# Kernel optimization log

Hardware: AMD Instinct MI355X
Metric: run time of the kernel (lower is better)

## Reference

```python
import jax, jax.numpy as jnp
import numpy as np

NUM_HEADS = 8
EPS = 1e-6


def setup_inputs() -> dict:
    key = jax.random.key(0)
    ks = jax.random.split(key, 6)
    B, C, H, W = 32, 512, 32, 32
    E = C
    scale = 1.0 / np.sqrt(E)
    x = jax.random.normal(ks[0], (B, C, H, W), dtype=jnp.float32)
    Wq = jax.random.normal(ks[1], (E, E), dtype=jnp.float32) * scale
    Wk = jax.random.normal(ks[2], (E, E), dtype=jnp.float32) * scale
    Wv = jax.random.normal(ks[3], (E, E), dtype=jnp.float32) * scale
    Wo = jax.random.normal(ks[4], (E, E), dtype=jnp.float32) * scale
    bo = jnp.zeros((E,), dtype=jnp.float32)
    return {"x": x, "Wq": Wq, "Wk": Wk, "Wv": Wv, "Wo": Wo, "bo": bo}


def reference(x, Wq, Wk, Wv, Wo, bo):
    B, C, H, W = x.shape
    S = H * W
    nh = NUM_HEADS
    hd = C // nh
    # (B, C, H, W) -> (B, S, C)
    t = x.reshape(B, C, S).transpose(0, 2, 1)
    # torch Linear: t @ W.T  (no bias for q/k/v)
    Q = (t @ Wq.T).reshape(B, S, nh, hd).transpose(0, 2, 1, 3)  # (B, nh, S, hd)
    K = (t @ Wk.T).reshape(B, S, nh, hd).transpose(0, 2, 1, 3)
    V = (t @ Wv.T).reshape(B, S, nh, hd).transpose(0, 2, 1, 3)
    phi_Q = jax.nn.elu(Q) + 1.0
    phi_K = jax.nn.elu(K) + 1.0
    # K^T V aggregation: (B, nh, hd, hd)
    KV = jnp.einsum('bhsd,bhse->bhde', phi_K, V)
    numerator = jnp.einsum('bhsd,bhde->bhse', phi_Q, KV)      # (B, nh, S, hd)
    # phi_K^T @ ones == sum over seq: (B, nh, hd)
    k_sum = jnp.sum(phi_K, axis=2)
    denominator = jnp.einsum('bhsd,bhd->bhs', phi_Q, k_sum)[..., None]  # (B, nh, S, 1)
    out = numerator / (denominator + EPS)
    out = out.transpose(0, 2, 1, 3).reshape(B, S, C)          # (B, S, C)
    out = out @ Wo.T + bo
    out = out.transpose(0, 2, 1).reshape(B, C, H, W)
    return out
```

## Files before the change

### kernel.cpp

```cpp
#include <hip/hip_runtime.h>
#include <hip/hip_bf16.h>

typedef __bf16 bf16;
typedef __bf16 bf16x2 __attribute__((ext_vector_type(2)));
typedef __bf16 bf16x4 __attribute__((ext_vector_type(4)));
typedef __bf16 bf16x8 __attribute__((ext_vector_type(8)));
typedef float  f32x4  __attribute__((ext_vector_type(4)));

#define MFMA16(a,b,c) __builtin_amdgcn_mfma_f32_16x16x32_bf16((a),(b),(c),0,0,0)

constexpr int Cn = 512;
constexpr int Sn = 1024;

__device__ __forceinline__ void bar_lds() {
    asm volatile("s_waitcnt lgkmcnt(0)" ::: "memory");
    __builtin_amdgcn_sched_barrier(0);
    __builtin_amdgcn_s_barrier();
}

__global__ __launch_bounds__(256) void k_cvt_w(const float* __restrict__ Wq,
                                               const float* __restrict__ Wk,
                                               const float* __restrict__ Wv,
                                               const float* __restrict__ Wo,
                                               bf16* __restrict__ Wb) {
    int tid = blockIdx.x * 256 + threadIdx.x;
    int oidx = tid * 8;
    int m  = oidx >> 18;
    int r  = oidx & 262143;
    int gr = r >> 13;
    int kc = (r >> 9) & 15;
    int l  = (r >> 3) & 63;
    const float* s = (m == 0) ? Wq : (m == 1) ? Wk : (m == 2) ? Wv : Wo;
    const float* src = s + (gr * 16 + (l & 15)) * 512 + kc * 32 + (l >> 4) * 8;
    float4 u = ((const float4*)src)[0], v = ((const float4*)src)[1];
    bf16x8 o;
    o[0] = (bf16)u.x; o[1] = (bf16)u.y; o[2] = (bf16)u.z; o[3] = (bf16)u.w;
    o[4] = (bf16)v.x; o[5] = (bf16)v.y; o[6] = (bf16)v.z; o[7] = (bf16)v.w;
    *(bf16x8*)(Wb + oidx) = o;
}

__global__ __launch_bounds__(1024, 4) void k_qkv(const float* __restrict__ x,
                                                 const bf16* __restrict__ Wb,
                                                 bf16* __restrict__ phiQ,
                                                 bf16* __restrict__ kvP,
                                                 float* __restrict__ ksP) {
    int bid = blockIdx.x;
    int st8 = bid & 7, b = bid >> 3;
    int t = threadIdx.x, lane = t & 63, w = t >> 6;
    int l15 = lane & 15, g = lane >> 4;
    int hq   = w >> 2;
    int quad = w & 3;

    __shared__ bf16 xT[64][520];
    __shared__ bf16 pk[4][64][72];
    __shared__ bf16 vv[4][64][72];
    __shared__ float ksl[512];

    if (t < 512) ksl[t] = 0.f;

    int rp = t >> 2;
    int sq = (t & 3) << 4;

    const float* xr0 = x + ((size_t)b * Cn + 2 * rp) * Sn + st8 * 128 + sq;
    {
        float4 f0[4], f1[4];
#pragma unroll
        for (int j = 0; j < 4; ++j) {
            f0[j] = ((const float4*)xr0)[j];
            f1[j] = ((const float4*)(xr0 + Sn))[j];
        }
#pragma unroll
        for (int j = 0; j < 4; ++j) {
            const float* e0 = (const float*)&f0[j];
            const float* e1 = (const float*)&f1[j];
#pragma unroll
            for (int e = 0; e < 4; ++e) {
                bf16x2 pr; pr[0] = (bf16)e0[e]; pr[1] = (bf16)e1[e];
                *(bf16x2*)&xT[sq + j * 4 + e][2 * rp] = pr;
            }
        }
    }
    float4 fB0[4], fB1[4];
#pragma unroll
    for (int j = 0; j < 4; ++j) {
        fB0[j] = ((const float4*)(xr0 + 64))[j];
        fB1[j] = ((const float4*)(xr0 + 64 + Sn))[j];
    }
    __syncthreads();

#pragma unroll 1
    for (int sub = 0; sub < 2; ++sub) {
        int srow0 = st8 * 128 + sub * 64;
#pragma unroll 1
        for (int rnd = 0; rnd < 2; ++rnd) {
            int h = rnd * 4 + hq;
            int gr = h * 4 + quad;
            f32x4 aQ[4], aK[4], aV[4];
#pragma unroll
            for (int n = 0; n < 4; ++n) {
                aQ[n] = (f32x4){0.f,0.f,0.f,0.f};
                aK[n] = (f32x4){0.f,0.f,0.f,0.f};
                aV[n] = (f32x4){0.f,0.f,0.f,0.f};
            }
            const bf16* wfQ = Wb + ((size_t)gr * 16) * 512 + lane * 8;
            const bf16* wfK = wfQ + (size_t)32 * 16 * 512;
            const bf16* wfV = wfQ + (size_t)64 * 16 * 512;
#pragma unroll 2
            for (int kc = 0; kc < 16; ++kc) {
                bf16x8 fq = *(const bf16x8*)(wfQ + kc * 512);
                bf16x8 fk = *(const bf16x8*)(wfK + kc * 512);
                bf16x8 fv = *(const bf16x8*)(wfV + kc * 512);
#pragma unroll
                for (int n = 0; n < 4; ++n) {
                    bf16x8 bf_ = *(const bf16x8*)&xT[n * 16 + l15][kc * 32 + g * 8];
                    aQ[n] = MFMA16(fq, bf_, aQ[n]);
                    aK[n] = MFMA16(fk, bf_, aK[n]);
                    aV[n] = MFMA16(fv, bf_, aV[n]);
                }
            }
            float kspart[4] = {0.f, 0.f, 0.f, 0.f};
#pragma unroll
            for (int n = 0; n < 4; ++n) {
                bf16x4 qv;
#pragma unroll
                for (int r = 0; r < 4; ++r) {
                    float kv_ = aK[n][r];
                    kv_ = kv_ > 0.f ? kv_ + 1.f : __expf(kv_);
                    bf16 kb = (bf16)kv_;
                    kspart[r] += (float)kb;
                    pk[hq][quad * 16 + g * 4 + r][n * 16 + l15] = kb;
                    vv[hq][quad * 16 + g * 4 + r][n * 16 + l15] = (bf16)aV[n][r];
                    float q = aQ[n][r];
                    q = q > 0.f ? q + 1.f : __expf(q);
                    qv[r] = (bf16)q;
                }
                *(bf16x4*)(phiQ + ((size_t)b * Sn + srow0 + n * 16 + l15) * Cn
                           + h * 64 + quad * 16 + g * 4) = qv;
            }
#pragma unroll
            for (int r = 0; r < 4; ++r) {
                float v = kspart[r];
                v += __shfl_xor(v, 1);
                v += __shfl_xor(v, 2);
                v += __shfl_xor(v, 4);
                v += __shfl_xor(v, 8);
                if (l15 == 0) ksl[h * 64 + quad * 16 + g * 4 + r] += v;
            }
            bar_lds();
            if (sub == 0 && rnd == 1) {
#pragma unroll
                for (int j = 0; j < 4; ++j) {
                    const float* e0 = (const float*)&fB0[j];
                    const float* e1 = (const float*)&fB1[j];
#pragma unroll
                    for (int e = 0; e < 4; ++e) {
                        bf16x2 pr; pr[0] = (bf16)e0[e]; pr[1] = (bf16)e1[e];
                        *(bf16x2*)&xT[sq + j * 4 + e][2 * rp] = pr;
                    }
                }
            }
            f32x4 kvacc[4];
#pragma unroll
            for (int n = 0; n < 4; ++n) kvacc[n] = (f32x4){0.f,0.f,0.f,0.f};
#pragma unroll
            for (int k2 = 0; k2 < 2; ++k2) {
                bf16x8 af = *(const bf16x8*)&pk[hq][quad * 16 + l15][k2 * 32 + g * 8];
#pragma unroll
                for (int n = 0; n < 4; ++n) {
                    bf16x8 bf_ = *(const bf16x8*)&vv[hq][n * 16 + l15][k2 * 32 + g * 8];
                    kvacc[n] = MFMA16(af, bf_, kvacc[n]);
                }
            }
            {
                bf16x8 p0, p1;
#pragma unroll
                for (int r = 0; r < 4; ++r) {
                    p0[r]     = (bf16)kvacc[0][r];
                    p0[4 + r] = (bf16)kvacc[1][r];
                    p1[r]     = (bf16)kvacc[2][r];
                    p1[4 + r] = (bf16)kvacc[3][r];
                }
                size_t base = ((size_t)((b * 8 + h) * 16 + st8 * 2 + sub)) * 4096;
                bf16* dst = kvP + base + (size_t)(quad * 64 + lane) * 16;
                *(bf16x8*)(dst)     = p0;
                *(bf16x8*)(dst + 8) = p1;
            }
            bar_lds();
        }
    }
    if (t < 512) {
        int h = t >> 6, d = t & 63;
        ksP[((b * 8 + h) * 8 + st8) * 64 + d] = ksl[t];
    }
}

__global__ __launch_bounds__(256) void k_red(const bf16* __restrict__ kvP,
                                             const float* __restrict__ ksP,
                                             bf16* __restrict__ KVT,
                                             float* __restrict__ ksum) {
    int bh = blockIdx.x;
    int t = threadIdx.x;
    int wq = t >> 6, lane = t & 63, g = lane >> 4, l15 = lane & 15;
    float acc[16];
#pragma unroll
    for (int i = 0; i < 16; ++i) acc[i] = 0.f;
#pragma unroll
    for (int p = 0; p < 16; ++p) {
        const bf16* src = kvP + ((size_t)bh * 16 + p) * 4096 + (size_t)t * 16;
        bf16x8 v0 = *(const bf16x8*)(src);
        bf16x8 v1 = *(const bf16x8*)(src + 8);
#pragma unroll
        for (int i = 0; i < 8; ++i) { acc[i] += (float)v0[i]; acc[8 + i] += (float)v1[i]; }
    }
#pragma unroll
    for (int n = 0; n < 4; ++n) {
        bf16x4 o;
#pragma unroll
        for (int r = 0; r < 4; ++r) o[r] = (bf16)acc[n * 4 + r];
        *(bf16x4*)(KVT + (size_t)bh * 4096 + (n * 16 + l15) * 64 + wq * 16 + g * 4) = o;
    }
    if (t < 64) {
        float s = 0.f;
#pragma unroll
        for (int p = 0; p < 8; ++p) s += ksP[((size_t)bh * 8 + p) * 64 + t];
        ksum[bh * 64 + t] = s;
    }
}

__global__ __launch_bounds__(1024, 4) void k_apply(const bf16* __restrict__ phiQ,
                                                   const bf16* __restrict__ Wb,
                                                   const bf16* __restrict__ KVT,
                                                   const float* __restrict__ ksum,
                                                   const float* __restrict__ bo,
                                                   float* __restrict__ out) {
    int bid = blockIdx.x;
    int st8 = bid & 7, b = bid >> 3;
    int t = threadIdx.x, lane = t & 63, w = t >> 6, l15 = lane & 15, g = lane >> 4;

    __shared__ bf16 pq[64][520];
    __shared__ float ksl[512];
    __shared__ float rden[64][8];
    __shared__ float bol[512];

    if (t < 512) {
        ksl[t] = ksum[b * 512 + t];
        bol[t] = bo[t];
    }

#pragma unroll 1
    for (int sub = 0; sub < 2; ++sub) {
        int srow0 = st8 * 128 + sub * 64;
        {
            int sr = t >> 4, c0 = (t & 15) * 32;
            const bf16* src = phiQ + ((size_t)b * Sn + srow0 + sr) * Cn + c0;
#pragma unroll
            for (int j = 0; j < 4; ++j)
                *(bf16x8*)&pq[sr][c0 + j * 8] = *(const bf16x8*)(src + j * 8);
        }
        __syncthreads();
        {
            int j = t >> 1, half = t & 1;
            int s = j & 63, h = j >> 6;
            float acc = 0.f;
#pragma unroll
            for (int dt = 0; dt < 4; ++dt) {
                bf16x8 v = *(const bf16x8*)&pq[s][h * 64 + half * 32 + dt * 8];
#pragma unroll
                for (int i = 0; i < 8; ++i)
                    acc += ksl[h * 64 + half * 32 + dt * 8 + i] * (float)v[i];
            }
            acc += __shfl_xor(acc, 1);
            if (half == 0) rden[s][h] = 1.f / (acc + 1e-6f);
        }
        __syncthreads();
        int h = w >> 1, eh = w & 1;
        f32x4 accN[2][4];
#pragma unroll
        for (int mi = 0; mi < 2; ++mi)
#pragma unroll
            for (int n = 0; n < 4; ++n) accN[mi][n] = (f32x4){0.f,0.f,0.f,0.f};
        {
            const bf16* kvb = KVT + ((size_t)(b * 8 + h)) * 4096;
#pragma unroll
            for (int k2 = 0; k2 < 2; ++k2) {
#pragma unroll
                for (int mi = 0; mi < 2; ++mi) {
                    bf16x8 af = *(const bf16x8*)(kvb + (eh * 32 + mi * 16 + l15) * 64 + k2 * 32 + g * 8);
#pragma unroll
                    for (int n = 0; n < 4; ++n) {
                        bf16x8 bf_ = *(const bf16x8*)&pq[n * 16 + l15][h * 64 + k2 * 32 + g * 8];
                        accN[mi][n] = MFMA16(af, bf_, accN[mi][n]);
                    }
                }
            }
        }
        __syncthreads();
#pragma unroll
        for (int mi = 0; mi < 2; ++mi)
#pragma unroll
            for (int n = 0; n < 4; ++n) {
                float rd = rden[n * 16 + l15][h];
                bf16x4 ov;
#pragma unroll
                for (int r = 0; r < 4; ++r) ov[r] = (bf16)(accN[mi][n][r] * rd);
                *(bf16x4*)&pq[n * 16 + l15][h * 64 + eh * 32 + mi * 16 + g * 4] = ov;
            }
        __syncthreads();
        int m0 = w * 32;
        f32x4 acc[2][4];
#pragma unroll
        for (int mi = 0; mi < 2; ++mi)
#pragma unroll
            for (int n = 0; n < 4; ++n) acc[mi][n] = (f32x4){0.f,0.f,0.f,0.f};
        const bf16* WoF = Wb + 786432 + (size_t)(w * 2) * 16 * 512 + lane * 8;
#pragma unroll 2
        for (int kc = 0; kc < 16; ++kc) {
            bf16x8 fa0 = *(const bf16x8*)(WoF + kc * 512);
            bf16x8 fa1 = *(const bf16x8*)(WoF + (16 + kc) * 512);
#pragma unroll
            for (int n = 0; n < 4; ++n) {
                bf16x8 bf_ = *(const bf16x8*)&pq[n * 16 + l15][kc * 32 + g * 8];
                acc[0][n] = MFMA16(fa0, bf_, acc[0][n]);
                acc[1][n] = MFMA16(fa1, bf_, acc[1][n]);
            }
        }
#pragma unroll
        for (int mi = 0; mi < 2; ++mi)
#pragma unroll
            for (int r = 0; r < 4; ++r) {
                int co = m0 + mi * 16 + g * 4 + r;
                float bb = bol[co];
#pragma unroll
                for (int n = 0; n < 4; ++n)
                    out[((size_t)b * Cn + co) * Sn + srow0 + n * 16 + l15] = acc[mi][n][r] + bb;
            }
        __syncthreads();
    }
}

extern "C" void kernel_launch(void* const* d_in, const int* in_sizes, int n_in,
                              void* d_out, int out_size, void* d_ws, size_t ws_size,
                              hipStream_t stream) {
    const float* x  = (const float*)d_in[0];
    const float* Wq = (const float*)d_in[1];
    const float* Wk = (const float*)d_in[2];
    const float* Wv = (const float*)d_in[3];
    const float* Wo = (const float*)d_in[4];
    const float* bo = (const float*)d_in[5];
    float* out = (float*)d_out;

    char* ws = (char*)d_ws;
    bf16*  phiQ = (bf16*)ws;
    bf16*  Wb   = (bf16*)(ws + 33554432);
    float* ksP  = (float*)(ws + 35651584);
    bf16*  KVT  = (bf16*)(ws + 36175872);
    float* ks   = (float*)(ws + 38273024);

    bf16*  kvP  = (bf16*)d_out;

    k_cvt_w <<< 512,  256, 0, stream>>>(Wq, Wk, Wv, Wo, Wb);
    k_qkv   <<< 256, 1024, 0, stream>>>(x, Wb, phiQ, kvP, ksP);
    k_red   <<< 256,  256, 0, stream>>>(kvP, ksP, KVT, ks);
    k_apply <<< 256, 1024, 0, stream>>>(phiQ, Wb, KVT, ks, bo, out);
}
```

Before: 116.0 us.

## Split QKV projection into smaller 512-thread blocks with swizzled LDS tiles

```diff
diff --git a/kernel.cpp b/kernel.cpp
--- a/kernel.cpp
+++ b/kernel.cpp
@@ -39,190 +39,187 @@
     *(bf16x8*)(Wb + oidx) = o;
 }
 
-__global__ __launch_bounds__(1024, 4) void k_qkv(const float* __restrict__ x,
-                                                 const bf16* __restrict__ Wb,
-                                                 bf16* __restrict__ phiQ,
-                                                 bf16* __restrict__ kvP,
-                                                 float* __restrict__ ksP) {
+__global__ __launch_bounds__(512, 4) void k_qkv(const float* __restrict__ x,
+                                                const bf16* __restrict__ Wb,
+                                                bf16* __restrict__ phiQ,
+                                                bf16* __restrict__ kvP,
+                                                float* __restrict__ ksP) {
     int bid = blockIdx.x;
-    int st8 = bid & 7, b = bid >> 3;
+    int st = bid & 15, b = bid >> 4;
     int t = threadIdx.x, lane = t & 63, w = t >> 6;
     int l15 = lane & 15, g = lane >> 4;
-    int hq   = w >> 2;
     int quad = w & 3;
-
-    __shared__ bf16 xT[64][520];
-    __shared__ bf16 pk[4][64][72];
-    __shared__ bf16 vv[4][64][72];
-    __shared__ float ksl[512];
-
-    if (t < 512) ksl[t] = 0.f;
-
-    int rp = t >> 2;
-    int sq = (t & 3) << 4;
-
-    const float* xr0 = x + ((size_t)b * Cn + 2 * rp) * Sn + st8 * 128 + sq;
+    int hh2  = w >> 2;
+
+    __shared__ bf16 xT[64 * 512];
+    __shared__ bf16 pkb[64 * 64];
+    __shared__ bf16 vvb[64 * 64];
+
     {
-        float4 f0[4], f1[4];
-#pragma unroll
-        for (int j = 0; j < 4; ++j) {
-            f0[j] = ((const float4*)xr0)[j];
-            f1[j] = ((const float4*)(xr0 + Sn))[j];
-        }
-#pragma unroll
-        for (int j = 0; j < 4; ++j) {
-            const float* e0 = (const float*)&f0[j];
-            const float* e1 = (const float*)&f1[j];
+        int rp = t >> 1;
+        int sh = (t & 1) * 32;
+        const float* xr = x + ((size_t)b * Cn + 2 * rp) * Sn + st * 64 + sh;
+#pragma unroll
+        for (int j = 0; j < 8; ++j) {
+            float4 a0 = ((const float4*)xr)[j];
+            float4 a1 = ((const float4*)(xr + Sn))[j];
+            const float* e0 = (const float*)&a0;
+            const float* e1 = (const float*)&a1;
 #pragma unroll
             for (int e = 0; e < 4; ++e) {
+                int s = sh + j * 4 + e;
                 bf16x2 pr; pr[0] = (bf16)e0[e]; pr[1] = (bf16)e1[e];
-                *(bf16x2*)&xT[sq + j * 4 + e][2 * rp] = pr;
-            }
-        }
-    }
-    float4 fB0[4], fB1[4];
-#pragma unroll
-    for (int j = 0; j < 4; ++j) {
-        fB0[j] = ((const float4*)(xr0 + 64))[j];
-        fB1[j] = ((const float4*)(xr0 + 64 + Sn))[j];
-    }
-    __syncthreads();
+                *(bf16x2*)&xT[s * 512 + (((rp >> 2) ^ (s & 7)) << 3) + 2 * (rp & 3)] = pr;
+            }
+        }
+    }
+    bar_lds();
 
 #pragma unroll 1
-    for (int sub = 0; sub < 2; ++sub) {
-        int srow0 = st8 * 128 + sub * 64;
+    for (int rnd = 0; rnd < 4; ++rnd) {
+        int h = rnd * 2 + hh2;
+        int gr = h * 4 + quad;
+        f32x4 aQ[4], aK[4], aV[4];
+#pragma unroll
+        for (int n = 0; n < 4; ++n) {
+            aQ[n] = (f32x4){0.f,0.f,0.f,0.f};
+            aK[n] = (f32x4){0.f,0.f,0.f,0.f};
+            aV[n] = (f32x4){0.f,0.f,0.f,0.f};
+        }
+        const bf16* wfQ = Wb + ((size_t)gr * 16) * 512 + lane * 8;
+        const bf16* wfK = wfQ + (size_t)32 * 16 * 512;
+        const bf16* wfV = wfQ + (size_t)64 * 16 * 512;
+#pragma unroll 2
+        for (int kc = 0; kc < 16; ++kc) {
+            bf16x8 fq = *(const bf16x8*)(wfQ + kc * 512);
+            bf16x8 fk = *(const bf16x8*)(wfK + kc * 512);
+            bf16x8 fv = *(const bf16x8*)(wfV + kc * 512);
+#pragma unroll
+            for (int n = 0; n < 4; ++n) {
+                bf16x8 bf_ = *(const bf16x8*)&xT[(n * 16 + l15) * 512
+                                                 + (((kc * 4 + g) ^ (l15 & 7)) << 3)];
+                aQ[n] = MFMA16(fq, bf_, aQ[n]);
+                aK[n] = MFMA16(fk, bf_, aK[n]);
+                aV[n] = MFMA16(fv, bf_, aV[n]);
+            }
+        }
+        bar_lds();
+        bf16x4 kbv[4], vbv[4];
+        float kspart[4] = {0.f, 0.f, 0.f, 0.f};
+#pragma unroll
+        for (int n = 0; n < 4; ++n) {
+            bf16x4 qv;
+#pragma unroll
+            for (int r = 0; r < 4; ++r) {
+                float kv_ = aK[n][r];
+                kv_ = kv_ > 0.f ? kv_ + 1.f : __expf(kv_);
+                bf16 kb = (bf16)kv_;
+                kspart[r] += (float)kb;
+                kbv[n][r] = kb;
+                vbv[n][r] = (bf16)aV[n][r];
+                float q = aQ[n][r];
+                q = q > 0.f ? q + 1.f : __expf(q);
+                qv[r] = (bf16)q;
+            }
+            *(bf16x4*)(phiQ + ((size_t)b * Sn + st * 64 + n * 16 + l15) * Cn
+                       + h * 64 + quad * 16 + g * 4) = qv;
+        }
+#pragma unroll
+        for (int r = 0; r < 4; ++r) {
+            float v = kspart[r];
+            v += __shfl_xor(v, 1);
+            v += __shfl_xor(v, 2);
+            v += __shfl_xor(v, 4);
+            v += __shfl_xor(v, 8);
+            if (l15 == 0)
+                ksP[((size_t)(b * 8 + h) * 16 + st) * 64 + quad * 16 + g * 4 + r] = v;
+        }
+        if (hh2 == 0) {
+#pragma unroll
+            for (int n = 0; n < 4; ++n)
+#pragma unroll
+                for (int r = 0; r < 4; ++r) {
+                    int d = quad * 16 + g * 4 + r;
+                    int soff = ((n * 2 + (l15 >> 3)) ^ (d & 7)) * 8 + (l15 & 7);
+                    pkb[d * 64 + soff] = kbv[n][r];
+                    vvb[d * 64 + soff] = vbv[n][r];
+                }
+        }
+        bar_lds();
 #pragma unroll 1
-        for (int rnd = 0; rnd < 2; ++rnd) {
-            int h = rnd * 4 + hq;
-            int gr = h * 4 + quad;
-            f32x4 aQ[4], aK[4], aV[4];
-#pragma unroll
-            for (int n = 0; n < 4; ++n) {
-                aQ[n] = (f32x4){0.f,0.f,0.f,0.f};
-                aK[n] = (f32x4){0.f,0.f,0.f,0.f};
-                aV[n] = (f32x4){0.f,0.f,0.f,0.f};
-            }
-            const bf16* wfQ = Wb + ((size_t)gr * 16) * 512 + lane * 8;
-            const bf16* wfK = wfQ + (size_t)32 * 16 * 512;
-            const bf16* wfV = wfQ + (size_t)64 * 16 * 512;
-#pragma unroll 2
-            for (int kc = 0; kc < 16; ++kc) {
-                bf16x8 fq = *(const bf16x8*)(wfQ + kc * 512);
-                bf16x8 fk = *(const bf16x8*)(wfK + kc * 512);
-                bf16x8 fv = *(const bf16x8*)(wfV + kc * 512);
-#pragma unroll
-                for (int n = 0; n < 4; ++n) {
-                    bf16x8 bf_ = *(const bf16x8*)&xT[n * 16 + l15][kc * 32 + g * 8];
-                    aQ[n] = MFMA16(fq, bf_, aQ[n]);
-                    aK[n] = MFMA16(fk, bf_, aK[n]);
-                    aV[n] = MFMA16(fv, bf_, aV[n]);
+        for (int hp = 0; hp < 2; ++hp) {
+            int quad_m = w & 3, eh = w >> 2;
+            f32x4 kv0 = (f32x4){0.f,0.f,0.f,0.f};
+            f32x4 kv1 = (f32x4){0.f,0.f,0.f,0.f};
+#pragma unroll
+            for (int k2 = 0; k2 < 2; ++k2) {
+                bf16x8 af = *(const bf16x8*)&pkb[(quad_m * 16 + l15) * 64
+                                                 + (((k2 * 4 + g) ^ (l15 & 7)) << 3)];
+                bf16x8 b0 = *(const bf16x8*)&vvb[(eh * 32 + l15) * 64
+                                                 + (((k2 * 4 + g) ^ (l15 & 7)) << 3)];
+                bf16x8 b1 = *(const bf16x8*)&vvb[(eh * 32 + 16 + l15) * 64
+                                                 + (((k2 * 4 + g) ^ (l15 & 7)) << 3)];
+                kv0 = MFMA16(af, b0, kv0);
+                kv1 = MFMA16(af, b1, kv1);
+            }
+            {
+                bf16x8 p;
+#pragma unroll
+                for (int r = 0; r < 4; ++r) {
+                    p[r]     = (bf16)kv0[r];
+                    p[4 + r] = (bf16)kv1[r];
                 }
-            }
-            float kspart[4] = {0.f, 0.f, 0.f, 0.f};
-#pragma unroll
-            for (int n = 0; n < 4; ++n) {
-                bf16x4 qv;
-#pragma unroll
-                for (int r = 0; r < 4; ++r) {
-                    float kv_ = aK[n][r];
-                    kv_ = kv_ > 0.f ? kv_ + 1.f : __expf(kv_);
-                    bf16 kb = (bf16)kv_;
-                    kspart[r] += (float)kb;
-                    pk[hq][quad * 16 + g * 4 + r][n * 16 + l15] = kb;
-                    vv[hq][quad * 16 + g * 4 + r][n * 16 + l15] = (bf16)aV[n][r];
-                    float q = aQ[n][r];
-                    q = q > 0.f ? q + 1.f : __expf(q);
-                    qv[r] = (bf16)q;
+                size_t base = ((size_t)((b * 8 + rnd * 2 + hp) * 16 + st)) * 4096;
+                *(bf16x8*)(kvP + base + (size_t)(w * 64 + lane) * 8) = p;
+            }
+            bar_lds();
+            if (hp == 0) {
+                if (hh2 == 1) {
+#pragma unroll
+                    for (int n = 0; n < 4; ++n)
+#pragma unroll
+                        for (int r = 0; r < 4; ++r) {
+                            int d = quad * 16 + g * 4 + r;
+                            int soff = ((n * 2 + (l15 >> 3)) ^ (d & 7)) * 8 + (l15 & 7);
+                            pkb[d * 64 + soff] = kbv[n][r];
+                            vvb[d * 64 + soff] = vbv[n][r];
+                        }
                 }
-                *(bf16x4*)(phiQ + ((size_t)b * Sn + srow0 + n * 16 + l15) * Cn
-                           + h * 64 + quad * 16 + g * 4) = qv;
-            }
-#pragma unroll
-            for (int r = 0; r < 4; ++r) {
-                float v = kspart[r];
-                v += __shfl_xor(v, 1);
-                v += __shfl_xor(v, 2);
-                v += __shfl_xor(v, 4);
-                v += __shfl_xor(v, 8);
-                if (l15 == 0) ksl[h * 64 + quad * 16 + g * 4 + r] += v;
-            }
-            bar_lds();
-            if (sub == 0 && rnd == 1) {
-#pragma unroll
-                for (int j = 0; j < 4; ++j) {
-                    const float* e0 = (const float*)&fB0[j];
-                    const float* e1 = (const float*)&fB1[j];
-#pragma unroll
-                    for (int e = 0; e < 4; ++e) {
-                        bf16x2 pr; pr[0] = (bf16)e0[e]; pr[1] = (bf16)e1[e];
-                        *(bf16x2*)&xT[sq + j * 4 + e][2 * rp] = pr;
-                    }
-                }
-            }
-            f32x4 kvacc[4];
-#pragma unroll
-            for (int n = 0; n < 4; ++n) kvacc[n] = (f32x4){0.f,0.f,0.f,0.f};
-#pragma unroll
-            for (int k2 = 0; k2 < 2; ++k2) {
-                bf16x8 af = *(const bf16x8*)&pk[hq][quad * 16 + l15][k2 * 32 + g * 8];
-#pragma unroll
-                for (int n = 0; n < 4; ++n) {
-                    bf16x8 bf_ = *(const bf16x8*)&vv[hq][n * 16 + l15][k2 * 32 + g * 8];
-                    kvacc[n] = MFMA16(af, bf_, kvacc[n]);
-                }
-            }
-            {
-                bf16x8 p0, p1;
-#pragma unroll
-                for (int r = 0; r < 4; ++r) {
-                    p0[r]     = (bf16)kvacc[0][r];
-                    p0[4 + r] = (bf16)kvacc[1][r];
-                    p1[r]     = (bf16)kvacc[2][r];
-                    p1[4 + r] = (bf16)kvacc[3][r];
-                }
-                size_t base = ((size_t)((b * 8 + h) * 16 + st8 * 2 + sub)) * 4096;
-                bf16* dst = kvP + base + (size_t)(quad * 64 + lane) * 16;
-                *(bf16x8*)(dst)     = p0;
-                *(bf16x8*)(dst + 8) = p1;
-            }
-            bar_lds();
-        }
-    }
-    if (t < 512) {
-        int h = t >> 6, d = t & 63;
-        ksP[((b * 8 + h) * 8 + st8) * 64 + d] = ksl[t];
-    }
-}
-
-__global__ __launch_bounds__(256) void k_red(const bf16* __restrict__ kvP,
+                bar_lds();
+            }
+        }
+    }
+}
+
+__global__ __launch_bounds__(512) void k_red(const bf16* __restrict__ kvP,
                                              const float* __restrict__ ksP,
                                              bf16* __restrict__ KVT,
                                              float* __restrict__ ksum) {
     int bh = blockIdx.x;
     int t = threadIdx.x;
-    int wq = t >> 6, lane = t & 63, g = lane >> 4, l15 = lane & 15;
-    float acc[16];
-#pragma unroll
-    for (int i = 0; i < 16; ++i) acc[i] = 0.f;
+    int w = t >> 6, lane = t & 63, g = lane >> 4, l15 = lane & 15;
+    int quad = w & 3, eh = w >> 2;
+    float acc[8];
+#pragma unroll
+    for (int i = 0; i < 8; ++i) acc[i] = 0.f;
 #pragma unroll
     for (int p = 0; p < 16; ++p) {
-        const bf16* src = kvP + ((size_t)bh * 16 + p) * 4096 + (size_t)t * 16;
-        bf16x8 v0 = *(const bf16x8*)(src);
-        bf16x8 v1 = *(const bf16x8*)(src + 8);
-#pragma unroll
-        for (int i = 0; i < 8; ++i) { acc[i] += (float)v0[i]; acc[8 + i] += (float)v1[i]; }
-    }
-#pragma unroll
-    for (int n = 0; n < 4; ++n) {
+        bf16x8 v = *(const bf16x8*)(kvP + ((size_t)bh * 16 + p) * 4096 + (size_t)t * 8);
+#pragma unroll
+        for (int i = 0; i < 8; ++i) acc[i] += (float)v[i];
+    }
+#pragma unroll
+    for (int n = 0; n < 2; ++n) {
         bf16x4 o;
 #pragma unroll
         for (int r = 0; r < 4; ++r) o[r] = (bf16)acc[n * 4 + r];
-        *(bf16x4*)(KVT + (size_t)bh * 4096 + (n * 16 + l15) * 64 + wq * 16 + g * 4) = o;
+        *(bf16x4*)(KVT + (size_t)bh * 4096 + (eh * 32 + n * 16 + l15) * 64
+                   + quad * 16 + g * 4) = o;
     }
     if (t < 64) {
         float s = 0.f;
 #pragma unroll
-        for (int p = 0; p < 8; ++p) s += ksP[((size_t)bh * 8 + p) * 64 + t];
+        for (int p = 0; p < 16; ++p) s += ksP[((size_t)bh * 16 + p) * 64 + t];
         ksum[bh * 64 + t] = s;
     }
 }
@@ -353,13 +350,13 @@
     bf16*  phiQ = (bf16*)ws;
     bf16*  Wb   = (bf16*)(ws + 33554432);
     float* ksP  = (float*)(ws + 35651584);
-    bf16*  KVT  = (bf16*)(ws + 36175872);
-    float* ks   = (float*)(ws + 38273024);
+    bf16*  KVT  = (bf16*)(ws + 36700160);
+    float* ks   = (float*)(ws + 38797312);
 
     bf16*  kvP  = (bf16*)d_out;
 
     k_cvt_w <<< 512,  256, 0, stream>>>(Wq, Wk, Wv, Wo, Wb);
-    k_qkv   <<< 256, 1024, 0, stream>>>(x, Wb, phiQ, kvP, ksP);
-    k_red   <<< 256,  256, 0, stream>>>(kvP, ksP, KVT, ks);
+    k_qkv   <<< 512,  512, 0, stream>>>(x, Wb, phiQ, kvP, ksP);
+    k_red   <<< 256,  512, 0, stream>>>(kvP, ksP, KVT, ks);
     k_apply <<< 256, 1024, 0, stream>>>(phiQ, Wb, KVT, ks, bo, out);
 }
```

After: 139.3 us. 1.2x slower.
